# Optimization experiments

Hardware: AMD Instinct MI355X
Metric: run time of the kernel (lower is better)

Reference implementation:

```python
import jax, jax.numpy as jnp
import numpy as np

NUM_ATOM_TYPES = 100
EMBED_DIM = 64
N_BATCH = 9000
ATOMS_PER_MOL = 64


def setup_inputs() -> dict:
    key = jax.random.key(0)
    k1, k2 = jax.random.split(key)
    atom_types = jax.random.randint(k1, (N_BATCH, ATOMS_PER_MOL), 0, NUM_ATOM_TYPES, dtype=jnp.int32)
    embedding = jax.random.normal(k2, (NUM_ATOM_TYPES, EMBED_DIM), dtype=jnp.float32)
    return {"atom_types": atom_types, "embedding": embedding}


def reference(atom_types, embedding):
    # Original: rank of each atom type within sorted unique values, then embed.
    flat = atom_types.reshape(-1)  # [N_BATCH*ATOMS_PER_MOL]
    # jit-friendly unique: pad with NUM_ATOM_TYPES (> any value) so array stays sorted
    uniq = jnp.unique(flat, size=NUM_ATOM_TYPES, fill_value=NUM_ATOM_TYPES)
    idx = jnp.searchsorted(uniq, flat)  # vectorized replacement for per-element jnp.where
    out = jnp.take(embedding, idx, axis=0)  # [total_atoms, EMBED_DIM]
    # jnp.split into n_batch equal chunks + stack == reshape
    return out.reshape(N_BATCH, -1, EMBED_DIM)
```

## Files before the change

### kernel.cpp

```cpp
#include <hip/hip_runtime.h>

#define NTYPES 100
#define EMBED 64
#define N_BATCH 9000
#define ATOMS_PER_MOL 64
#define N_ATOMS (N_BATCH * ATOMS_PER_MOL)

__global__ void ae_zero_present(int* __restrict__ present) {
    if (threadIdx.x < 128) present[threadIdx.x] = 0;
}

__global__ void ae_mark_present(const int4* __restrict__ at4,
                                int* __restrict__ present, int n4) {
    int stride = gridDim.x * blockDim.x;
    for (int i = blockIdx.x * blockDim.x + threadIdx.x; i < n4; i += stride) {
        int4 v = at4[i];
        present[v.x] = 1;
        present[v.y] = 1;
        present[v.z] = 1;
        present[v.w] = 1;
    }
}

__global__ void ae_build_remap(const int* __restrict__ present,
                               const float* __restrict__ embedding,
                               float* __restrict__ remap) {
    __shared__ int s_present[NTYPES];
    __shared__ int s_rank[NTYPES];
    int tid = threadIdx.x;
    if (tid < NTYPES) s_present[tid] = present[tid];
    __syncthreads();
    if (tid < NTYPES) {
        int r = 0;
        for (int j = 0; j < tid; ++j) r += s_present[j];
        s_rank[tid] = r;
    }
    __syncthreads();
    for (int idx = tid; idx < NTYPES * EMBED; idx += blockDim.x) {
        int t = idx >> 6;
        int d = idx & 63;
        remap[idx] = embedding[s_rank[t] * EMBED + d];
    }
}

__global__ void ae_gather(const int* __restrict__ atom_types,
                          const float4* __restrict__ remap4,
                          float4* __restrict__ out4, int total) {
    int stride = gridDim.x * blockDim.x;
    for (int g = blockIdx.x * blockDim.x + threadIdx.x; g < total; g += stride) {
        int i = g >> 4;
        int q = g & 15;
        int t = atom_types[i];
        out4[g] = remap4[t * 16 + q];
    }
}

extern "C" void kernel_launch(void* const* d_in, const int* in_sizes, int n_in,
                              void* d_out, int out_size, void* d_ws, size_t ws_size,
                              hipStream_t stream) {
    const int* atom_types    = (const int*)d_in[0];
    const float* embedding   = (const float*)d_in[1];
    float* out               = (float*)d_out;

    int*   present = (int*)d_ws;
    float* remap   = (float*)((char*)d_ws + 512);

    ae_zero_present<<<1, 128, 0, stream>>>(present);

    int n4 = N_ATOMS / 4;
    ae_mark_present<<<1024, 256, 0, stream>>>((const int4*)atom_types, present, n4);

    ae_build_remap<<<1, 256, 0, stream>>>(present, embedding, remap);

    int total = N_ATOMS * 16;
    ae_gather<<<2048, 256, 0, stream>>>(atom_types, (const float4*)remap,
                                        (float4*)out, total);
}
```

Measured before the change: 45.78 us.

## Fuse rank computation into gather kernel and drop remap table

The separate remap-building kernel is removed. Each gather block now loads the presence flags, computes per-type ranks in shared memory, and gathers directly from the embedding table. The zero kernel becomes a memset, and the mark kernel runs with one thread per int4 instead of a grid-stride loop. This cuts one launch and one serial dependency, at the cost of every block redoing a small rank prefix computation.

```diff
diff --git a/kernel.cpp b/kernel.cpp
--- a/kernel.cpp
+++ b/kernel.cpp
@@ -5,15 +5,12 @@
 #define N_BATCH 9000
 #define ATOMS_PER_MOL 64
 #define N_ATOMS (N_BATCH * ATOMS_PER_MOL)
-
-__global__ void ae_zero_present(int* __restrict__ present) {
-    if (threadIdx.x < 128) present[threadIdx.x] = 0;
-}
+#define TOTAL4 (N_ATOMS * 16)
 
 __global__ void ae_mark_present(const int4* __restrict__ at4,
                                 int* __restrict__ present, int n4) {
-    int stride = gridDim.x * blockDim.x;
-    for (int i = blockIdx.x * blockDim.x + threadIdx.x; i < n4; i += stride) {
+    int i = blockIdx.x * blockDim.x + threadIdx.x;
+    if (i < n4) {
         int4 v = at4[i];
         present[v.x] = 1;
         present[v.y] = 1;
@@ -22,9 +19,11 @@
     }
 }
 
-__global__ void ae_build_remap(const int* __restrict__ present,
-                               const float* __restrict__ embedding,
-                               float* __restrict__ remap) {
+__global__ __launch_bounds__(256) void ae_gather(
+        const int* __restrict__ atom_types,
+        const float4* __restrict__ emb4,
+        const int* __restrict__ present,
+        float4* __restrict__ out4) {
     __shared__ int s_present[NTYPES];
     __shared__ int s_rank[NTYPES];
     int tid = threadIdx.x;
@@ -36,43 +35,30 @@
         s_rank[tid] = r;
     }
     __syncthreads();
-    for (int idx = tid; idx < NTYPES * EMBED; idx += blockDim.x) {
-        int t = idx >> 6;
-        int d = idx & 63;
-        remap[idx] = embedding[s_rank[t] * EMBED + d];
-    }
-}
 
-__global__ void ae_gather(const int* __restrict__ atom_types,
-                          const float4* __restrict__ remap4,
-                          float4* __restrict__ out4, int total) {
     int stride = gridDim.x * blockDim.x;
-    for (int g = blockIdx.x * blockDim.x + threadIdx.x; g < total; g += stride) {
-        int i = g >> 4;
-        int q = g & 15;
-        int t = atom_types[i];
-        out4[g] = remap4[t * 16 + q];
+    for (int g = blockIdx.x * blockDim.x + tid; g < TOTAL4; g += stride) {
+        int t = atom_types[g >> 4];
+        int r = s_rank[t];
+        out4[g] = emb4[r * 16 + (g & 15)];
     }
 }
 
 extern "C" void kernel_launch(void* const* d_in, const int* in_sizes, int n_in,
                               void* d_out, int out_size, void* d_ws, size_t ws_size,
                               hipStream_t stream) {
-    const int* atom_types    = (const int*)d_in[0];
-    const float* embedding   = (const float*)d_in[1];
-    float* out               = (float*)d_out;
+    const int* atom_types  = (const int*)d_in[0];
+    const float* embedding = (const float*)d_in[1];
+    float* out             = (float*)d_out;
 
-    int*   present = (int*)d_ws;
-    float* remap   = (float*)((char*)d_ws + 512);
+    int* present = (int*)d_ws;
 
-    ae_zero_present<<<1, 128, 0, stream>>>(present);
+    hipMemsetAsync(present, 0, 512, stream);
 
     int n4 = N_ATOMS / 4;
-    ae_mark_present<<<1024, 256, 0, stream>>>((const int4*)atom_types, present, n4);
+    ae_mark_present<<<(n4 + 255) / 256, 256, 0, stream>>>(
+        (const int4*)atom_types, present, n4);
 
-    ae_build_remap<<<1, 256, 0, stream>>>(present, embedding, remap);
-
-    int total = N_ATOMS * 16;
-    ae_gather<<<2048, 256, 0, stream>>>(atom_types, (const float4*)remap,
-                                        (float4*)out, total);
+    ae_gather<<<2048, 256, 0, stream>>>(atom_types, (const float4*)embedding,
+                                        present, (float4*)out);
 }
```

Result: faster. 38.57 us (-15.8%).
